# Optimization experiments

Hardware: AMD Instinct MI355X
Metric: run time of the kernel (lower is better)

The kernel has to match this reference:

```python
import jax, jax.numpy as jnp
import numpy as np
from jax import lax

C, H, W, N = 128, 48, 48, 16
SHIFT_W = 1   # frozen value of p_3_1_1 (random.randint(-3,3) in original)
SHIFT_C = 1   # frozen value of p_11_0_1


def setup_inputs() -> dict:
    key = jax.random.key(0)
    k1, k2, k3, k4, k5 = jax.random.split(key, 5)
    x = jax.random.normal(k1, (N, C, H, W), dtype=jnp.float32)
    # p_5_w: trunc_normal std=0.02, shape (1,c,h,w)
    p5_w = 0.02 * jax.random.truncated_normal(k2, -2.0, 2.0, (1, C, H, W), dtype=jnp.float32)
    # p_6: 1x1 conv c->c, no bias -> weight (c, c)
    w6 = jax.random.normal(k3, (C, C), dtype=jnp.float32) / np.float32(np.sqrt(C))
    # p_8: Conv2d(1, c//2, (1,5), dilation=(1,3), padding=(0,6), bias=False)
    w8 = jax.random.normal(k4, (C // 2, 1, 1, 5), dtype=jnp.float32) / np.float32(np.sqrt(5))
    # p_10: 1x1 conv 3c/2 -> c, no bias
    w10 = jax.random.normal(k5, (C, 3 * C // 2), dtype=jnp.float32) / np.float32(np.sqrt(3 * C // 2))
    return {"x": x, "p5_w": p5_w, "w6": w6, "w8": w8, "w10": w10}


def _forward(x, p5_w, w6, w8, w10):
    n, c, h, w = x.shape
    hw = h * w
    inv_sqrt_c = np.float32(1.0 / np.sqrt(c))
    inv_sqrt_hw = np.float32(1.0 / np.sqrt(hw))

    t1 = x.max(axis=1)                                    # (n,h,w) channel max
    t2 = -x
    t4 = jnp.maximum(t2, jnp.roll(t2, SHIFT_W, axis=3))    # roll along width
    t5 = p5_w * t4
    t6 = jnp.einsum('oc,nchw->nohw', w6, t5)               # 1x1 conv p_6

    # score tensor t_7: (n, hw, hw)
    t7 = jnp.einsum('ncp,ncq->npq', t6.reshape(n, c, hw), x.reshape(n, c, hw)) * inv_sqrt_c

    # dilated 1x5 conv on channel-max map
    t8 = lax.conv_general_dilated(
        t1[:, None, :, :], w8, window_strides=(1, 1),
        padding=((0, 0), (6, 6)), rhs_dilation=(1, 3),
        dimension_numbers=('NCHW', 'OIHW', 'NCHW'))        # (n, c/2, h, w)

    # unfold kernel (3,1), dilation (2,1), padding (2,0): rows i-2, i, i+2
    pad = jnp.pad(t8, ((0, 0), (0, 0), (2, 2), (0, 0)))
    t9 = jnp.stack([pad[:, :, 2 * k:2 * k + h, :] for k in range(3)], axis=2)  # (n,c/2,3,h,w)

    t10 = jnp.einsum('oc,nchw->nohw', w10, t9.reshape(n, 3 * c // 2, h, w))   # 1x1 conv p_10
    t11 = jnp.roll(t10, SHIFT_C, axis=1)                   # roll along channels
    t12 = jnp.maximum(x, t11)

    # out[n,q,c] = sum_p t7[n,p,q] * t12[n,c,p]
    t13 = jnp.einsum('npq,ncp->nqc', t7, t12.reshape(n, c, hw)) * inv_sqrt_hw
    return t13.reshape(n, h, w, c).transpose(0, 3, 1, 2)   # (n,c,h,w)


def reference(x, p5_w, w6, w8, w10):
    return _forward(x, p5_w, w6, w8, w10)
```

## Files before the change

### kernel.cpp

```cpp
#include <hip/hip_runtime.h>
#include <cmath>

typedef short bf16x8 __attribute__((ext_vector_type(8)));
typedef short bf16x4 __attribute__((ext_vector_type(4)));
typedef float f32x4 __attribute__((ext_vector_type(4)));

namespace {
constexpr int kN   = 16;
constexpr int kC   = 128;
constexpr int kH   = 48;
constexpr int kW   = 48;
constexpr int kHW  = kH * kW;
constexpr int kK9  = 192;
constexpr int kNPC = 18;
constexpr int kPCH = kHW / kNPC;
constexpr int kLS  = 132;
constexpr int kPA  = 136;
}

__device__ __forceinline__ unsigned short f2b(float f) {
  unsigned u = __builtin_bit_cast(unsigned, f);
  u = (u + 0x7FFFu + ((u >> 16) & 1u)) >> 16;
  return (unsigned short)u;
}
__device__ __forceinline__ float b2f(unsigned short u) {
  return __builtin_bit_cast(float, ((unsigned)u) << 16);
}

__device__ __forceinline__ int tidx(int w, int c) {
  return w * kLS + (c ^ (((w >> 2) & 3) << 3));
}

__global__ __launch_bounds__(256)
void k_prep(const float* __restrict__ p5, const float* __restrict__ w6,
            const float* __restrict__ w10, const float* __restrict__ w8,
            float* __restrict__ p5T, unsigned short* __restrict__ w6b,
            float* __restrict__ Weff) {
  const int tid = threadIdx.x;
  const int bb = blockIdx.x;
  if (bb < 48) {
    __shared__ float Ls[kW * kLS];
    const int h = bb;
    for (int i = 0; i < 6; ++i) {
      const int idx = i * 256 + tid;
      const int c = idx / 12, s = idx % 12;
      const float4 v = *(const float4*)(p5 + (size_t)c * kHW + h * kW + s * 4);
      const int sw = (s & 3) << 3;
      Ls[(4 * s + 0) * kLS + (c ^ sw)] = v.x;
      Ls[(4 * s + 1) * kLS + (c ^ sw)] = v.y;
      Ls[(4 * s + 2) * kLS + (c ^ sw)] = v.z;
      Ls[(4 * s + 3) * kLS + (c ^ sw)] = v.w;
    }
    __syncthreads();
    for (int i = 0; i < 3; ++i) {
      const int idx = i * 256 + tid;
      const int w = idx >> 4, c = (idx & 15) * 8;
      const float* s = &Ls[tidx(w, c)];
      float4 a{s[0], s[1], s[2], s[3]}, b{s[4], s[5], s[6], s[7]};
      float* dst = p5T + ((size_t)(h * kW + w)) * kC + c;
      *(float4*)dst = a;
      *(float4*)(dst + 4) = b;
    }
  } else if (bb < 112) {
    const int i = (bb - 48) * 256 + tid;
    w6b[i] = f2b(w6[i]);
  } else {
    const int idx = (bb - 112) * 256 + tid;
    if (idx < kC * 15) {
      const int o = idx / 15, t = idx - o * 15;
      const int kk = t / 5, j = t - kk * 5;
      float s = 0.f;
#pragma unroll
      for (int c2 = 0; c2 < 64; ++c2)
        s = fmaf(w10[o * kK9 + 3 * c2 + kk], w8[c2 * 5 + j], s);
      Weff[idx] = s;
    }
  }
}

__global__ __launch_bounds__(256)
void k_xt5t6(const float* __restrict__ x, const float* __restrict__ p5T,
             const unsigned short* __restrict__ w6b,
             unsigned short* __restrict__ xT, unsigned short* __restrict__ xB,
             float* __restrict__ t1, unsigned short* __restrict__ t6) {
  __shared__ __align__(16) float Ls[kW * kLS];
  __shared__ __align__(16) unsigned short t5s[kW * kPA];
  const int b = blockIdx.x;
  const int n = b / kH, h = b - n * kH;
  const int tid = threadIdx.x;
  const float* xrow = x + (size_t)n * kC * kHW + h * kW;
  unsigned short* xBrow = xB + (size_t)n * kC * kHW + h * kW;
  for (int i = 0; i < 6; ++i) {
    const int idx = i * 256 + tid;
    const int c = idx / 12, s = idx % 12;
    const float4 v = *(const float4*)(xrow + (size_t)c * kHW + s * 4);
    const int sw = (s & 3) << 3;
    Ls[(4 * s + 0) * kLS + (c ^ sw)] = v.x;
    Ls[(4 * s + 1) * kLS + (c ^ sw)] = v.y;
    Ls[(4 * s + 2) * kLS + (c ^ sw)] = v.z;
    Ls[(4 * s + 3) * kLS + (c ^ sw)] = v.w;
    bf16x4 xb4{(short)f2b(v.x), (short)f2b(v.y), (short)f2b(v.z), (short)f2b(v.w)};
    *(bf16x4*)(xBrow + (size_t)c * kHW + s * 4) = xb4;
  }
  __syncthreads();

  for (int i = 0; i < 3; ++i) {
    const int idx = i * 256 + tid;
    const int w = idx >> 4, c = (idx & 15) * 8;
    const int wp = (w == 0) ? (kW - 1) : (w - 1);
    const float* sv = &Ls[tidx(w, c)];
    const float* sp = &Ls[tidx(wp, c)];
    const int q = h * kW + w;
    const float* pv = p5T + (size_t)q * kC + c;

    unsigned short xb[8], tb[8];
    float m = -3.4e38f;
#pragma unroll
    for (int j = 0; j < 8; ++j) {
      const float xv = sv[j];
      const float t5 = pv[j] * fmaxf(-xv, -sp[j]);
      xb[j] = f2b(xv);
      tb[j] = f2b(t5);
      m = fmaxf(m, xv);
    }
    *(bf16x8*)(xT + ((size_t)n * kHW + q) * kC + c) = *(const bf16x8*)xb;
    *(bf16x8*)&t5s[w * kPA + c] = *(const bf16x8*)tb;
#pragma unroll
    for (int off = 1; off < 16; off <<= 1)
      m = fmaxf(m, __shfl_xor(m, off, 16));
    if ((tid & 15) == 0) t1[(size_t)n * kHW + q] = m;
  }
  __syncthreads();

  const int wv = tid >> 6, lane = tid & 63;
  const int lr = lane & 15, lk = (lane >> 4) * 8;
  f32x4 acc[2][3];
#pragma unroll
  for (int i = 0; i < 2; ++i)
#pragma unroll
    for (int j = 0; j < 3; ++j) acc[i][j] = f32x4{0.f, 0.f, 0.f, 0.f};
#pragma unroll
  for (int ks = 0; ks < kC; ks += 32) {
    bf16x8 a[2], bf[3];
#pragma unroll
    for (int mt = 0; mt < 2; ++mt)
      a[mt] = *(const bf16x8*)(w6b + (size_t)(32 * wv + 16 * mt + lr) * kC + ks + lk);
#pragma unroll
    for (int nt = 0; nt < 3; ++nt)
      bf[nt] = *(const bf16x8*)&t5s[(16 * nt + lr) * kPA + ks + lk];
#pragma unroll
    for (int mt = 0; mt < 2; ++mt)
#pragma unroll
      for (int nt = 0; nt < 3; ++nt)
        acc[mt][nt] = __builtin_amdgcn_mfma_f32_16x16x32_bf16(a[mt], bf[nt], acc[mt][nt], 0, 0, 0);
  }
#pragma unroll
  for (int mt = 0; mt < 2; ++mt)
#pragma unroll
    for (int nt = 0; nt < 3; ++nt) {
      const int q = h * kW + 16 * nt + lr;
#pragma unroll
      for (int r = 0; r < 4; ++r) {
        const int o = 32 * wv + 16 * mt + 4 * (lane >> 4) + r;
        t6[((size_t)n * kC + o) * kHW + q] = f2b(acc[mt][nt][r]);
      }
    }
}

__global__ __launch_bounds__(256)
void k_corr(const unsigned short* __restrict__ xB, const float* __restrict__ t1,
            const float* __restrict__ Weff, const unsigned short* __restrict__ t6,
            unsigned short* __restrict__ part) {
  __shared__ __align__(16) unsigned short t12s[kC * kPA];
  __shared__ __align__(16) unsigned short Bsf[kC * kPA];
  __shared__ __align__(16) float t1s[8 * 60];
  __shared__ float sW[kC][15];
  const int tid = threadIdx.x;
  const int n = blockIdx.y;
  const int chunk = blockIdx.x;
  const int p0 = chunk * kPCH;
  const int h_lo = p0 / kW;
  const unsigned short* Bg = t6 + (size_t)n * kC * kHW + p0;

  for (int i = tid; i < 8 * 60; i += 256) {
    const int r = i / 60, cc = i - r * 60;
    const int hh = h_lo - 2 + r, ww = cc - 6;
    t1s[i] = (hh >= 0 && hh < kH && ww >= 0 && ww < kW) ? t1[n * kHW + hh * kW + ww] : 0.f;
  }
  for (int i = tid; i < kC * 15; i += 256) {
    const int c = i / 15, t = i - c * 15;
    sW[c][t] = Weff[((c - 1) & (kC - 1)) * 15 + t];
  }
#pragma unroll
  for (int i = 0; i < 8; ++i) {
    const int f = i * 256 + tid;
    const int c = f >> 4, seg = (f & 15) * 8;
    *(bf16x8*)&Bsf[c * kPA + seg] = *(const bf16x8*)(Bg + (size_t)c * kHW + seg);
  }
  __syncthreads();

  const unsigned short* xn = xB + (size_t)n * kC * kHW;
  for (int it = 0; it < 8; ++it) {
    const int idx = it * 256 + tid;
    const int c = idx >> 4, p = (idx & 15) * 8;
    const int q = p0 + p;
    const int h = q / kW, w0 = q - h * kW;
    const int r0 = h - h_lo;
    float tap[3][20];
#pragma unroll
    for (int kk = 0; kk < 3; ++kk) {
      const float* src = &t1s[(r0 + 2 * kk) * 60 + w0];
#pragma unroll
      for (int j4 = 0; j4 < 5; ++j4) {
        const float4 v = *(const float4*)(src + 4 * j4);
        tap[kk][4 * j4 + 0] = v.x; tap[kk][4 * j4 + 1] = v.y;
        tap[kk][4 * j4 + 2] = v.z; tap[kk][4 * j4 + 3] = v.w;
      }
    }
    float wr[15];
#pragma unroll
    for (int t = 0; t < 15; ++t) wr[t] = sW[c][t];
    const bf16x8 xv8 = *(const bf16x8*)(xn + (size_t)c * kHW + q);
    unsigned short o16[8];
#pragma unroll
    for (int dp = 0; dp < 8; ++dp) {
      float acc = 0.f;
#pragma unroll
      for (int kk = 0; kk < 3; ++kk)
#pragma unroll
        for (int j = 0; j < 5; ++j)
          acc = fmaf(wr[kk * 5 + j], tap[kk][3 * j + dp], acc);
      o16[dp] = f2b(fmaxf(b2f((unsigned short)xv8[dp]), acc));
    }
    *(bf16x8*)&t12s[c * kPA + p] = *(const bf16x8*)o16;
  }
  __syncthreads();

  const int wv = tid >> 6, lane = tid & 63;
  const int lr = lane & 15, lk = (lane >> 4) * 8;
  const int wr2 = (wv >> 1) * 64, wc2 = (wv & 1) * 64;
  f32x4 acc[4][4];
#pragma unroll
  for (int i = 0; i < 4; ++i)
#pragma unroll
    for (int j = 0; j < 4; ++j) acc[i][j] = f32x4{0.f, 0.f, 0.f, 0.f};

#pragma unroll
  for (int ks = 0; ks < kPCH; ks += 32) {
    bf16x8 a[4], bv[4];
#pragma unroll
    for (int i = 0; i < 4; ++i) {
      a[i]  = *(const bf16x8*)&t12s[(wr2 + 16 * i + lr) * kPA + ks + lk];
      bv[i] = *(const bf16x8*)&Bsf[(wc2 + 16 * i + lr) * kPA + ks + lk];
    }
#pragma unroll
    for (int i = 0; i < 4; ++i)
#pragma unroll
      for (int j = 0; j < 4; ++j)
        acc[i][j] = __builtin_amdgcn_mfma_f32_16x16x32_bf16(a[i], bv[j], acc[i][j], 0, 0, 0);
  }

  unsigned short* dst = part + ((size_t)chunk * kN + n) * (kC * kC);
#pragma unroll
  for (int i = 0; i < 4; ++i)
#pragma unroll
    for (int j = 0; j < 4; ++j)
#pragma unroll
      for (int r = 0; r < 4; ++r)
        dst[(wr2 + 16 * i + 4 * (lane >> 4) + r) * kC + wc2 + 16 * j + lr] = f2b(acc[i][j][r]);
}

__global__ __launch_bounds__(256)
void k_redM(const unsigned short* __restrict__ part, unsigned short* __restrict__ M) {
  const int bid = blockIdx.x;
  const int j = bid >> 4, n = bid & 15;
  const int r0 = (j * 256 + threadIdx.x) * 8;
  float acc[8];
#pragma unroll
  for (int e = 0; e < 8; ++e) acc[e] = 0.f;
#pragma unroll
  for (int ch = 0; ch < kNPC; ++ch) {
    const bf16x8 v = *(const bf16x8*)(part + (((size_t)ch * kN + n) << 14) + r0);
#pragma unroll
    for (int e = 0; e < 8; ++e) acc[e] += b2f((unsigned short)v[e]);
  }
  unsigned short o16[8];
#pragma unroll
  for (int e = 0; e < 8; ++e) o16[e] = f2b(acc[e]);
  *(bf16x8*)(M + ((size_t)n << 14) + r0) = *(const bf16x8*)o16;
}

__global__ __launch_bounds__(256)
void k_out(const unsigned short* __restrict__ A, const unsigned short* __restrict__ B,
           float* __restrict__ Out, float scale) {
  constexpr int K = 128;
  __shared__ __align__(16) unsigned short Bs[64 * kPA];
  const int tid = threadIdx.x;
  const int n = blockIdx.y;
  const int qbase = blockIdx.x * 64;
  const unsigned short* Ag = A + (size_t)n * kC * K;
  const unsigned short* Bg = B + ((size_t)n * kHW + qbase) * K;

#pragma unroll
  for (int i = 0; i < 4; ++i) {
    const int f = i * 256 + tid;
    const int q = f >> 4, seg = (f & 15) * 8;
    *(bf16x8*)&Bs[q * kPA + seg] = *(const bf16x8*)(Bg + (size_t)q * K + seg);
  }
  __syncthreads();

  const int wv = tid >> 6, lane = tid & 63;
  const int lr = lane & 15, lk = (lane >> 4) * 8;

  f32x4 acc[2][4];
#pragma unroll
  for (int i = 0; i < 2; ++i)
#pragma unroll
    for (int j = 0; j < 4; ++j) acc[i][j] = f32x4{0.f, 0.f, 0.f, 0.f};

#pragma unroll
  for (int ks = 0; ks < K; ks += 32) {
    bf16x8 a[2], b[4];
#pragma unroll
    for (int mt = 0; mt < 2; ++mt)
      a[mt] = *(const bf16x8*)(Ag + (size_t)(32 * wv + 16 * mt + lr) * K + ks + lk);
#pragma unroll
    for (int nt = 0; nt < 4; ++nt)
      b[nt] = *(const bf16x8*)&Bs[(16 * nt + lr) * kPA + ks + lk];
#pragma unroll
    for (int mt = 0; mt < 2; ++mt)
#pragma unroll
      for (int nt = 0; nt < 4; ++nt)
        acc[mt][nt] = __builtin_amdgcn_mfma_f32_16x16x32_bf16(
            a[mt], b[nt], acc[mt][nt], 0, 0, 0);
  }

#pragma unroll
  for (int mt = 0; mt < 2; ++mt)
#pragma unroll
    for (int nt = 0; nt < 4; ++nt) {
      const int q = qbase + 16 * nt + lr;
#pragma unroll
      for (int r = 0; r < 4; ++r) {
        const int m = 32 * wv + 16 * mt + 4 * (lane >> 4) + r;
        Out[((size_t)n * kC + m) * kHW + q] = scale * acc[mt][nt][r];
      }
    }
}

extern "C" void kernel_launch(void* const* d_in, const int* in_sizes, int n_in,
                              void* d_out, int out_size, void* d_ws, size_t ws_size,
                              hipStream_t stream) {
  const float* x   = (const float*)d_in[0];
  const float* p5  = (const float*)d_in[1];
  const float* w6  = (const float*)d_in[2];
  const float* w8  = (const float*)d_in[3];
  const float* w10 = (const float*)d_in[4];
  float* out = (float*)d_out;

  char* ws = (char*)d_ws;
  unsigned short* xT   = (unsigned short*)(ws);
  unsigned short* t6b  = (unsigned short*)(ws + 9437184);
  unsigned short* part = (unsigned short*)(ws + 18874368);
  unsigned short* xB   = (unsigned short*)(ws + 28311552);
  unsigned short* Mb   = (unsigned short*)(ws + 37748736);
  float*          t1b  = (float*)(ws + 38273024);
  unsigned short* w6b  = (unsigned short*)(ws + 38420480);
  float*          Weff = (float*)(ws + 38453248);
  float*          p5T  = (float*)(ws + 38460928);

  const float scale = 1.0f / (sqrtf((float)kC) * sqrtf((float)kHW));

  k_prep<<<120, 256, 0, stream>>>(p5, w6, w10, w8, p5T, w6b, Weff);
  k_xt5t6<<<kN * kH, 256, 0, stream>>>(x, p5T, w6b, xT, xB, t1b, t6b);
  k_corr<<<dim3(kNPC, kN), 256, 0, stream>>>(xB, t1b, Weff, t6b, part);
  k_redM<<<8 * kN, 256, 0, stream>>>(part, Mb);
  k_out<<<dim3(kHW / 64, kN), 256, 0, stream>>>(Mb, xT, out, scale);
}
```

Baseline: 47.67 us.

## Compute dilated conv plus 1x1 projection via MFMA and stream t6 from global

The fused 15-tap dilated conv and channel projection (Weff) that builds t12 moves from per-thread scalar FMAs onto a bf16 MFMA GEMM. Weff is stored as bf16 padded to K=32, and the 15 taps per position go into a small LDS tile. The t6 operand for the correlation GEMM is now read directly from global memory instead of being staged in LDS. This frees LDS and drops the scalar conv loop, but the conv weights and taps are now rounded to bf16 and the GEMM B loads go uncoalesced through global or L2.

```diff
diff --git a/kernel.cpp b/kernel.cpp
--- a/kernel.cpp
+++ b/kernel.cpp
@@ -16,6 +16,7 @@
 constexpr int kPCH = kHW / kNPC;
 constexpr int kLS  = 132;
 constexpr int kPA  = 136;
+constexpr int kTB  = 40;
 }
 
 __device__ __forceinline__ unsigned short f2b(float f) {
@@ -35,7 +36,7 @@
 void k_prep(const float* __restrict__ p5, const float* __restrict__ w6,
             const float* __restrict__ w10, const float* __restrict__ w8,
             float* __restrict__ p5T, unsigned short* __restrict__ w6b,
-            float* __restrict__ Weff) {
+            unsigned short* __restrict__ WeffR) {
   const int tid = threadIdx.x;
   const int bb = blockIdx.x;
   if (bb < 48) {
@@ -66,15 +67,16 @@
     w6b[i] = f2b(w6[i]);
   } else {
     const int idx = (bb - 112) * 256 + tid;
-    if (idx < kC * 15) {
-      const int o = idx / 15, t = idx - o * 15;
-      const int kk = t / 5, j = t - kk * 5;
-      float s = 0.f;
+    const int c = idx >> 5, t = idx & 31;
+    float s = 0.f;
+    if (t < 15) {
+      const int o = (c - 1) & (kC - 1);
+      const int kk = t / 5, j = t - 5 * kk;
 #pragma unroll
       for (int c2 = 0; c2 < 64; ++c2)
         s = fmaf(w10[o * kK9 + 3 * c2 + kk], w8[c2 * 5 + j], s);
-      Weff[idx] = s;
-    }
+    }
+    WeffR[idx] = f2b(s);
   }
 }
 
@@ -169,76 +171,92 @@
 
 __global__ __launch_bounds__(256)
 void k_corr(const unsigned short* __restrict__ xB, const float* __restrict__ t1,
-            const float* __restrict__ Weff, const unsigned short* __restrict__ t6,
+            const unsigned short* __restrict__ WeffR, const unsigned short* __restrict__ t6,
             unsigned short* __restrict__ part) {
   __shared__ __align__(16) unsigned short t12s[kC * kPA];
-  __shared__ __align__(16) unsigned short Bsf[kC * kPA];
+  __shared__ __align__(16) unsigned short tapB[kPCH * kTB];
   __shared__ __align__(16) float t1s[8 * 60];
-  __shared__ float sW[kC][15];
   const int tid = threadIdx.x;
   const int n = blockIdx.y;
   const int chunk = blockIdx.x;
   const int p0 = chunk * kPCH;
   const int h_lo = p0 / kW;
-  const unsigned short* Bg = t6 + (size_t)n * kC * kHW + p0;
 
   for (int i = tid; i < 8 * 60; i += 256) {
     const int r = i / 60, cc = i - r * 60;
     const int hh = h_lo - 2 + r, ww = cc - 6;
     t1s[i] = (hh >= 0 && hh < kH && ww >= 0 && ww < kW) ? t1[n * kHW + hh * kW + ww] : 0.f;
   }
-  for (int i = tid; i < kC * 15; i += 256) {
-    const int c = i / 15, t = i - c * 15;
-    sW[c][t] = Weff[((c - 1) & (kC - 1)) * 15 + t];
-  }
-#pragma unroll
-  for (int i = 0; i < 8; ++i) {
-    const int f = i * 256 + tid;
-    const int c = f >> 4, seg = (f & 15) * 8;
-    *(bf16x8*)&Bsf[c * kPA + seg] = *(const bf16x8*)(Bg + (size_t)c * kHW + seg);
-  }
-  __syncthreads();
-
-  const unsigned short* xn = xB + (size_t)n * kC * kHW;
-  for (int it = 0; it < 8; ++it) {
-    const int idx = it * 256 + tid;
-    const int c = idx >> 4, p = (idx & 15) * 8;
-    const int q = p0 + p;
-    const int h = q / kW, w0 = q - h * kW;
-    const int r0 = h - h_lo;
-    float tap[3][20];
-#pragma unroll
-    for (int kk = 0; kk < 3; ++kk) {
-      const float* src = &t1s[(r0 + 2 * kk) * 60 + w0];
-#pragma unroll
-      for (int j4 = 0; j4 < 5; ++j4) {
-        const float4 v = *(const float4*)(src + 4 * j4);
-        tap[kk][4 * j4 + 0] = v.x; tap[kk][4 * j4 + 1] = v.y;
-        tap[kk][4 * j4 + 2] = v.z; tap[kk][4 * j4 + 3] = v.w;
+  __syncthreads();
+
+  {
+    const int p = tid >> 1, o8 = (tid & 1) * 8;
+    const int q = p0 + p, h = q / kW, w = q - h * kW, r0 = h - h_lo;
+    unsigned short tv[8];
+#pragma unroll
+    for (int e = 0; e < 8; ++e) {
+      const int t = o8 + e;
+      float v = 0.f;
+      if (t < 15) {
+        const int kk = t / 5, j = t - 5 * kk;
+        v = t1s[(r0 + 2 * kk) * 60 + w + 3 * j];
       }
-    }
-    float wr[15];
-#pragma unroll
-    for (int t = 0; t < 15; ++t) wr[t] = sW[c][t];
-    const bf16x8 xv8 = *(const bf16x8*)(xn + (size_t)c * kHW + q);
-    unsigned short o16[8];
-#pragma unroll
-    for (int dp = 0; dp < 8; ++dp) {
-      float acc = 0.f;
-#pragma unroll
-      for (int kk = 0; kk < 3; ++kk)
-#pragma unroll
-        for (int j = 0; j < 5; ++j)
-          acc = fmaf(wr[kk * 5 + j], tap[kk][3 * j + dp], acc);
-      o16[dp] = f2b(fmaxf(b2f((unsigned short)xv8[dp]), acc));
-    }
-    *(bf16x8*)&t12s[c * kPA + p] = *(const bf16x8*)o16;
+      tv[e] = f2b(v);
+    }
+    *(bf16x8*)&tapB[p * kTB + o8] = *(const bf16x8*)tv;
+    const unsigned short z[8] = {0, 0, 0, 0, 0, 0, 0, 0};
+    *(bf16x8*)&tapB[p * kTB + 16 + o8] = *(const bf16x8*)z;
   }
   __syncthreads();
 
   const int wv = tid >> 6, lane = tid & 63;
   const int lr = lane & 15, lk = (lane >> 4) * 8;
   const int wr2 = (wv >> 1) * 64, wc2 = (wv & 1) * 64;
+
+  {
+    f32x4 acc2[4][4];
+#pragma unroll
+    for (int i = 0; i < 4; ++i)
+#pragma unroll
+      for (int j = 0; j < 4; ++j) acc2[i][j] = f32x4{0.f, 0.f, 0.f, 0.f};
+    bf16x8 a2[4], b2[4];
+#pragma unroll
+    for (int i = 0; i < 4; ++i) {
+      a2[i] = *(const bf16x8*)(WeffR + (size_t)(wr2 + 16 * i + lr) * 32 + lk);
+      b2[i] = *(const bf16x8*)&tapB[(wc2 + 16 * i + lr) * kTB + lk];
+    }
+#pragma unroll
+    for (int i = 0; i < 4; ++i)
+#pragma unroll
+      for (int j = 0; j < 4; ++j)
+        acc2[i][j] = __builtin_amdgcn_mfma_f32_16x16x32_bf16(a2[i], b2[j], acc2[i][j], 0, 0, 0);
+#pragma unroll
+    for (int i = 0; i < 4; ++i)
+#pragma unroll
+      for (int j = 0; j < 4; ++j)
+#pragma unroll
+        for (int r = 0; r < 4; ++r)
+          t12s[(wr2 + 16 * i + 4 * (lane >> 4) + r) * kPA + wc2 + 16 * j + lr] =
+              f2b(acc2[i][j][r]);
+  }
+  __syncthreads();
+
+  const unsigned short* xn = xB + (size_t)n * kC * kHW;
+#pragma unroll
+  for (int it = 0; it < 8; ++it) {
+    const int idx = it * 256 + tid;
+    const int c = idx >> 4, po = (idx & 15) * 8;
+    bf16x8 tv = *(bf16x8*)&t12s[c * kPA + po];
+    const bf16x8 xv = *(const bf16x8*)(xn + (size_t)c * kHW + p0 + po);
+    unsigned short o16[8];
+#pragma unroll
+    for (int e = 0; e < 8; ++e)
+      o16[e] = f2b(fmaxf(b2f((unsigned short)tv[e]), b2f((unsigned short)xv[e])));
+    *(bf16x8*)&t12s[c * kPA + po] = *(const bf16x8*)o16;
+  }
+  __syncthreads();
+
+  const unsigned short* t6g = t6 + (size_t)n * kC * kHW + p0;
   f32x4 acc[4][4];
 #pragma unroll
   for (int i = 0; i < 4; ++i)
@@ -251,7 +269,7 @@
 #pragma unroll
     for (int i = 0; i < 4; ++i) {
       a[i]  = *(const bf16x8*)&t12s[(wr2 + 16 * i + lr) * kPA + ks + lk];
-      bv[i] = *(const bf16x8*)&Bsf[(wc2 + 16 * i + lr) * kPA + ks + lk];
+      bv[i] = *(const bf16x8*)(t6g + (size_t)(wc2 + 16 * i + lr) * kHW + ks + lk);
     }
 #pragma unroll
     for (int i = 0; i < 4; ++i)
@@ -359,21 +377,21 @@
   float* out = (float*)d_out;
 
   char* ws = (char*)d_ws;
-  unsigned short* xT   = (unsigned short*)(ws);
-  unsigned short* t6b  = (unsigned short*)(ws + 9437184);
-  unsigned short* part = (unsigned short*)(ws + 18874368);
-  unsigned short* xB   = (unsigned short*)(ws + 28311552);
-  unsigned short* Mb   = (unsigned short*)(ws + 37748736);
-  float*          t1b  = (float*)(ws + 38273024);
-  unsigned short* w6b  = (unsigned short*)(ws + 38420480);
-  float*          Weff = (float*)(ws + 38453248);
-  float*          p5T  = (float*)(ws + 38460928);
+  unsigned short* xT    = (unsigned short*)(ws);
+  unsigned short* t6b   = (unsigned short*)(ws + 9437184);
+  unsigned short* part  = (unsigned short*)(ws + 18874368);
+  unsigned short* xB    = (unsigned short*)(ws + 28311552);
+  unsigned short* Mb    = (unsigned short*)(ws + 37748736);
+  float*          t1b   = (float*)(ws + 38273024);
+  unsigned short* w6b   = (unsigned short*)(ws + 38420480);
+  unsigned short* WeffR = (unsigned short*)(ws + 38453248);
+  float*          p5T   = (float*)(ws + 38461440);
 
   const float scale = 1.0f / (sqrtf((float)kC) * sqrtf((float)kHW));
 
-  k_prep<<<120, 256, 0, stream>>>(p5, w6, w10, w8, p5T, w6b, Weff);
+  k_prep<<<128, 256, 0, stream>>>(p5, w6, w10, w8, p5T, w6b, WeffR);
   k_xt5t6<<<kN * kH, 256, 0, stream>>>(x, p5T, w6b, xT, xB, t1b, t6b);
-  k_corr<<<dim3(kNPC, kN), 256, 0, stream>>>(xB, t1b, Weff, t6b, part);
+  k_corr<<<dim3(kNPC, kN), 256, 0, stream>>>(xB, t1b, WeffR, t6b, part);
   k_redM<<<8 * kN, 256, 0, stream>>>(part, Mb);
   k_out<<<dim3(kHW / 64, kN), 256, 0, stream>>>(Mb, xT, out, scale);
 }
```

After: 46.98 us. About the same (-1.5%).
